# Kernel tuning notes

Hardware: AMD Instinct MI355X
Metric: run time of the kernel (lower is better)

Reference implementation:

```python
import jax, jax.numpy as jnp
import numpy as np


def setup_inputs() -> dict:
    key = jax.random.key(0)
    k1, k2, k3 = jax.random.split(key, 3)
    B, N, Lq, Ld, D = 32, 8, 256, 512, 768
    questions = jax.random.normal(k1, (B, Lq, D), dtype=jnp.float32)
    docs = jax.random.normal(k2, (B, N, Ld, D), dtype=jnp.float32)
    is_ans = jax.random.randint(k3, (B, N), 0, 2).astype(jnp.bool_)
    return {"questions": questions, "docs": docs, "is_ans": is_ans}


def reference(questions, docs, is_ans):
    # questions: [B, Lq, D]; docs: [B, N, Ld, D]; is_ans: [B, N] bool
    q_mean = questions.mean(axis=1)        # [B, D]
    d_mean = docs.mean(axis=2)             # [B, N, D]
    sim = jnp.einsum('bd,bnd->bn', q_mean, d_mean)  # [B, N]
    # loss -= sim where is_ans else loss += sim
    sign = jnp.where(is_ans, -1.0, 1.0).astype(sim.dtype)
    loss = jnp.sum(sign * sim)
    return loss
```

## Files before the change

kernel.cpp:

```cpp
#include <hip/hip_runtime.h>

#define BB 32
#define NN 8
#define LQ 256
#define LD 512
#define DD 768
#define D4 (DD / 4)

#define QCH 8
#define QROWS (LQ / QCH)
#define QPART_F4 (QCH * BB * D4)
#define CH 8
#define LCHUNK (LD / CH)
#define NBLK (BB * NN * CH)

typedef float f4 __attribute__((ext_vector_type(4)));

__global__ void __launch_bounds__(192)
qsum_kernel(const f4* __restrict__ q, f4* __restrict__ qpart,
            unsigned* __restrict__ counter) {
    int blk = blockIdx.x;
    int b = blk >> 3;
    int c = blk & 7;
    int t = threadIdx.x;
    if (blk == 0 && t == 0) *counter = 0u;

    const f4* p = q + ((size_t)b * LQ + (size_t)c * QROWS) * D4 + t;
    f4 a0 = 0.f, a1 = 0.f, a2 = 0.f, a3 = 0.f;
    f4 a4 = 0.f, a5 = 0.f, a6 = 0.f, a7 = 0.f;
#pragma unroll
    for (int i = 0; i < QROWS; i += 8) {
        a0 += p[(size_t)(i + 0) * D4];
        a1 += p[(size_t)(i + 1) * D4];
        a2 += p[(size_t)(i + 2) * D4];
        a3 += p[(size_t)(i + 3) * D4];
        a4 += p[(size_t)(i + 4) * D4];
        a5 += p[(size_t)(i + 5) * D4];
        a6 += p[(size_t)(i + 6) * D4];
        a7 += p[(size_t)(i + 7) * D4];
    }
    qpart[((size_t)c * BB + b) * D4 + t] = ((a0 + a1) + (a2 + a3)) + ((a4 + a5) + (a6 + a7));
}

__global__ void __launch_bounds__(192)
docs_kernel(const f4* __restrict__ docs4, const int* __restrict__ is_ans,
            const f4* __restrict__ qpart, float* __restrict__ partials,
            unsigned* __restrict__ counter, float* __restrict__ out) {
    int bn    = blockIdx.x >> 3;
    int chunk = blockIdx.x & 7;
    int b     = bn >> 3;
    int t     = threadIdx.x;

    f4 qv = 0.f;
#pragma unroll
    for (int c = 0; c < QCH; ++c)
        qv += qpart[((size_t)c * BB + b) * D4 + t];

    const f4* p = docs4 + ((size_t)bn * LD + (size_t)chunk * LCHUNK) * D4 + t;
    f4 acc = 0.f;
#pragma unroll 8
    for (int l = 0; l < LCHUNK; ++l) {
        f4 v = __builtin_nontemporal_load(&p[(size_t)l * D4]);
        acc += v * qv;
    }
    float s = acc.x + acc.y + acc.z + acc.w;

    for (int off = 32; off > 0; off >>= 1)
        s += __shfl_down(s, off, 64);

    __shared__ float wsum[3];
    __shared__ int amLast;
    if ((t & 63) == 0) wsum[t >> 6] = s;
    __syncthreads();
    if (t == 0) {
        float sign = is_ans[bn] ? -1.f : 1.f;
        partials[blockIdx.x] = (wsum[0] + wsum[1] + wsum[2]) * sign;
        __threadfence();
        unsigned old = atomicAdd(counter, 1u);
        amLast = (old == NBLK - 1);
    }
    __syncthreads();
    if (amLast) {
        __threadfence();
        float s2 = 0.f;
        for (int i = t; i < NBLK; i += 192)
            s2 += partials[i];
        for (int off = 32; off > 0; off >>= 1)
            s2 += __shfl_down(s2, off, 64);
        __shared__ float w2[3];
        if ((t & 63) == 0) w2[t >> 6] = s2;
        __syncthreads();
        if (t == 0)
            out[0] = (w2[0] + w2[1] + w2[2]) * (1.f / ((float)LQ * (float)LD));
    }
}

extern "C" void kernel_launch(void* const* d_in, const int* in_sizes, int n_in,
                              void* d_out, int out_size, void* d_ws, size_t ws_size,
                              hipStream_t stream) {
    const f4*  q      = (const f4*)d_in[0];
    const f4*  docs4  = (const f4*)d_in[1];
    const int* is_ans = (const int*)d_in[2];
    float* out = (float*)d_out;

    f4*       qpart    = (f4*)d_ws;
    float*    partials = (float*)(qpart + QPART_F4);
    unsigned* counter  = (unsigned*)(partials + NBLK);

    qsum_kernel<<<dim3(BB * QCH), 192, 0, stream>>>(q, qpart, counter);
    docs_kernel<<<dim3(NBLK), 192, 0, stream>>>(docs4, is_ans, qpart, partials, counter, out);
}
```

Baseline: 596.6 us.

## Stream question and doc sums in one kernel, then dot in finish kernel

Moves the question-sum blocks and the doc-sum blocks into a single launch, so the doc stream no longer waits on the question reduction and the two can overlap. Doc blocks now store signed per-chunk column sums in place of dot products, and a small finish kernel with 32 blocks forms the dot product and accumulates into the output with an atomic add. This drops the counter/last-block reduction and the nontemporal loads, but adds a write and re-read of the doc partials (about 4.7 MB). It also relies on out being zeroed by block 0 before any finish block runs, which the kernel boundary guarantees.

Measured after the change: 538.7 us. 1.11x faster.

```diff
diff --git a/kernel.cpp b/kernel.cpp
--- a/kernel.cpp
+++ b/kernel.cpp
@@ -9,90 +9,86 @@
 
 #define QCH 8
 #define QROWS (LQ / QCH)
+#define QBLKS (BB * QCH)
 #define QPART_F4 (QCH * BB * D4)
+
 #define CH 8
 #define LCHUNK (LD / CH)
-#define NBLK (BB * NN * CH)
+#define DBLKS (BB * NN * CH)
+#define DPART_F4 (DBLKS * D4)
 
 typedef float f4 __attribute__((ext_vector_type(4)));
 
 __global__ void __launch_bounds__(192)
-qsum_kernel(const f4* __restrict__ q, f4* __restrict__ qpart,
-            unsigned* __restrict__ counter) {
+stream_kernel(const f4* __restrict__ q, const f4* __restrict__ docs4,
+              const int* __restrict__ is_ans,
+              f4* __restrict__ qpart, f4* __restrict__ dpart,
+              float* __restrict__ out) {
     int blk = blockIdx.x;
-    int b = blk >> 3;
-    int c = blk & 7;
-    int t = threadIdx.x;
-    if (blk == 0 && t == 0) *counter = 0u;
+    int t   = threadIdx.x;
 
-    const f4* p = q + ((size_t)b * LQ + (size_t)c * QROWS) * D4 + t;
-    f4 a0 = 0.f, a1 = 0.f, a2 = 0.f, a3 = 0.f;
-    f4 a4 = 0.f, a5 = 0.f, a6 = 0.f, a7 = 0.f;
+    if (blk < QBLKS) {
+        int b = blk >> 3;
+        int c = blk & 7;
+        if (blk == 0 && t == 0) out[0] = 0.f;
+        const f4* p = q + ((size_t)b * LQ + (size_t)c * QROWS) * D4 + t;
+        f4 a0 = 0.f, a1 = 0.f, a2 = 0.f, a3 = 0.f;
+        f4 a4 = 0.f, a5 = 0.f, a6 = 0.f, a7 = 0.f;
 #pragma unroll
-    for (int i = 0; i < QROWS; i += 8) {
-        a0 += p[(size_t)(i + 0) * D4];
-        a1 += p[(size_t)(i + 1) * D4];
-        a2 += p[(size_t)(i + 2) * D4];
-        a3 += p[(size_t)(i + 3) * D4];
-        a4 += p[(size_t)(i + 4) * D4];
-        a5 += p[(size_t)(i + 5) * D4];
-        a6 += p[(size_t)(i + 6) * D4];
-        a7 += p[(size_t)(i + 7) * D4];
+        for (int i = 0; i < QROWS; i += 8) {
+            a0 += p[(size_t)(i + 0) * D4];
+            a1 += p[(size_t)(i + 1) * D4];
+            a2 += p[(size_t)(i + 2) * D4];
+            a3 += p[(size_t)(i + 3) * D4];
+            a4 += p[(size_t)(i + 4) * D4];
+            a5 += p[(size_t)(i + 5) * D4];
+            a6 += p[(size_t)(i + 6) * D4];
+            a7 += p[(size_t)(i + 7) * D4];
+        }
+        qpart[((size_t)c * BB + b) * D4 + t] =
+            ((a0 + a1) + (a2 + a3)) + ((a4 + a5) + (a6 + a7));
+    } else {
+        int idx   = blk - QBLKS;
+        int bn    = idx >> 3;
+        int chunk = idx & 7;
+        const f4* p = docs4 + ((size_t)bn * LD + (size_t)chunk * LCHUNK) * D4 + t;
+        f4 acc0 = 0.f, acc1 = 0.f;
+#pragma unroll 4
+        for (int l = 0; l < LCHUNK; l += 2) {
+            acc0 += p[(size_t)(l + 0) * D4];
+            acc1 += p[(size_t)(l + 1) * D4];
+        }
+        float sign = is_ans[bn] ? -1.f : 1.f;
+        dpart[(size_t)idx * D4 + t] = (acc0 + acc1) * sign;
     }
-    qpart[((size_t)c * BB + b) * D4 + t] = ((a0 + a1) + (a2 + a3)) + ((a4 + a5) + (a6 + a7));
 }
 
 __global__ void __launch_bounds__(192)
-docs_kernel(const f4* __restrict__ docs4, const int* __restrict__ is_ans,
-            const f4* __restrict__ qpart, float* __restrict__ partials,
-            unsigned* __restrict__ counter, float* __restrict__ out) {
-    int bn    = blockIdx.x >> 3;
-    int chunk = blockIdx.x & 7;
-    int b     = bn >> 3;
-    int t     = threadIdx.x;
+finish_kernel(const f4* __restrict__ qpart, const f4* __restrict__ dpart,
+              float* __restrict__ out) {
+    int b = blockIdx.x;
+    int t = threadIdx.x;
 
     f4 qv = 0.f;
 #pragma unroll
     for (int c = 0; c < QCH; ++c)
         qv += qpart[((size_t)c * BB + b) * D4 + t];
 
-    const f4* p = docs4 + ((size_t)bn * LD + (size_t)chunk * LCHUNK) * D4 + t;
-    f4 acc = 0.f;
+    f4 dv = 0.f;
 #pragma unroll 8
-    for (int l = 0; l < LCHUNK; ++l) {
-        f4 v = __builtin_nontemporal_load(&p[(size_t)l * D4]);
-        acc += v * qv;
-    }
-    float s = acc.x + acc.y + acc.z + acc.w;
+    for (int i = 0; i < NN * CH; ++i)
+        dv += dpart[(size_t)(b * NN * CH + i) * D4 + t];
 
+    f4 m = qv * dv;
+    float s = m.x + m.y + m.z + m.w;
     for (int off = 32; off > 0; off >>= 1)
         s += __shfl_down(s, off, 64);
 
     __shared__ float wsum[3];
-    __shared__ int amLast;
     if ((t & 63) == 0) wsum[t >> 6] = s;
     __syncthreads();
-    if (t == 0) {
-        float sign = is_ans[bn] ? -1.f : 1.f;
-        partials[blockIdx.x] = (wsum[0] + wsum[1] + wsum[2]) * sign;
-        __threadfence();
-        unsigned old = atomicAdd(counter, 1u);
-        amLast = (old == NBLK - 1);
-    }
-    __syncthreads();
-    if (amLast) {
-        __threadfence();
-        float s2 = 0.f;
-        for (int i = t; i < NBLK; i += 192)
-            s2 += partials[i];
-        for (int off = 32; off > 0; off >>= 1)
-            s2 += __shfl_down(s2, off, 64);
-        __shared__ float w2[3];
-        if ((t & 63) == 0) w2[t >> 6] = s2;
-        __syncthreads();
-        if (t == 0)
-            out[0] = (w2[0] + w2[1] + w2[2]) * (1.f / ((float)LQ * (float)LD));
-    }
+    if (t == 0)
+        atomicAdd(out, (wsum[0] + wsum[1] + wsum[2]) * (1.f / ((float)LQ * (float)LD)));
 }
 
 extern "C" void kernel_launch(void* const* d_in, const int* in_sizes, int n_in,
@@ -103,10 +99,9 @@
     const int* is_ans = (const int*)d_in[2];
     float* out = (float*)d_out;
 
-    f4*       qpart    = (f4*)d_ws;
-    float*    partials = (float*)(qpart + QPART_F4);
-    unsigned* counter  = (unsigned*)(partials + NBLK);
+    f4* qpart = (f4*)d_ws;
+    f4* dpart = qpart + QPART_F4;
 
-    qsum_kernel<<<dim3(BB * QCH), 192, 0, stream>>>(q, qpart, counter);
-    docs_kernel<<<dim3(NBLK), 192, 0, stream>>>(docs4, is_ans, qpart, partials, counter, out);
+    stream_kernel<<<dim3(QBLKS + DBLKS), 192, 0, stream>>>(q, docs4, is_ans, qpart, dpart, out);
+    finish_kernel<<<dim3(BB), 192, 0, stream>>>(qpart, dpart, out);
 }
```
